# Optimization experiments

Hardware: AMD Instinct MI355X
Metric: run time of the kernel (lower is better)

Reference implementation:

```python
import jax, jax.numpy as jnp
import numpy as np

K = 32          # neighbors
DIV = 4         # division
S = K // DIV    # maxpool window
EPS = 1e-5      # BatchNorm eps (torch default)


def _bn_last(x, g, b):
    # BatchNorm over channel = last axis, training-mode batch stats (biased var),
    # equivalent to torch's transpose->BatchNorm2d->transpose in Dense(in_dim=4).
    m = x.mean(axis=(0, 1, 2), keepdims=True)
    v = x.var(axis=(0, 1, 2), keepdims=True)
    return (x - m) / jnp.sqrt(v + EPS) * g + b


def setup_inputs() -> dict:
    key = jax.random.key(0)
    ks = jax.random.split(key, 16)
    B, N, M, F1, F2 = 8, 4096, 2048, 128, 256
    Fmid = 64
    Cin = Fmid + F1  # 192
    inp = {
        "points": jax.random.normal(ks[0], (B, N, 3), dtype=jnp.float32),
        "queries": jax.random.normal(ks[1], (B, M, 3), dtype=jnp.float32),
        "prev_features": jax.random.normal(ks[2], (B, N, F1), dtype=jnp.float32),
        # dense1: 3 -> 32
        "g1": jnp.ones((3,), jnp.float32),
        "b1": jnp.zeros((3,), jnp.float32),
        "W1": jax.random.normal(ks[3], (3, Fmid // 2), dtype=jnp.float32) * 0.3,
        "c1": jnp.zeros((Fmid // 2,), jnp.float32),
        # dense2: 32 -> 64
        "g2": jnp.ones((Fmid // 2,), jnp.float32),
        "b2": jnp.zeros((Fmid // 2,), jnp.float32),
        "W2": jax.random.normal(ks[4], (Fmid // 2, Fmid), dtype=jnp.float32) * 0.1,
        "c2": jnp.zeros((Fmid,), jnp.float32),
        # conv block: BN2d(192) + Conv2d(192 -> 256, kernel (1,4))
        "g3": jnp.ones((Cin,), jnp.float32),
        "b3": jnp.zeros((Cin,), jnp.float32),
        "Wc": jax.random.normal(ks[5], (F2, Cin, DIV), dtype=jnp.float32) * 0.05,
        "bc": jnp.zeros((F2,), jnp.float32),
    }
    return inp


def reference(points, queries, prev_features, g1, b1, W1, c1, g2, b2, W2, c2,
              g3, b3, Wc, bc):
    B, N, _ = points.shape
    M = queries.shape[1]

    # --- KNN: negative squared distance, topk largest = k nearest ---
    # dist[b,m,n] = -||q-p||^2 = 2 q.p - ||q||^2 - ||p||^2
    dist = (2.0 * jnp.einsum('bmd,bnd->bmn', queries, points)
            - jnp.sum(queries ** 2, -1)[:, :, None]
            - jnp.sum(points ** 2, -1)[:, None, :])
    _, idx = jax.lax.top_k(dist, K)  # (B, M, K) int32

    gather = jax.vmap(lambda feats, i: feats[i])  # (N,F),(M,K) -> (M,K,F)
    knn_pts = gather(points, idx)                 # (B, M, K, 3)

    # local coords: center - neighbor
    local = queries[:, :, None, :] - knn_pts       # (B, M, K, 3)

    # dense1 / dense2: BN -> Linear -> ReLU
    h = jax.nn.relu(_bn_last(local, g1, b1) @ W1 + c1)  # (B,M,K,32)
    h = jax.nn.relu(_bn_last(h, g2, b2) @ W2 + c2)      # (B,M,K,64)

    # gather previous features, concat
    prev_k = gather(prev_features, idx)                 # (B,M,K,F1)
    feat = jnp.concatenate([h, prev_k], axis=-1)        # (B,M,K,192)

    # permute to NCHW, maxpool (1,S) stride S over K -> width DIV
    x = jnp.transpose(feat, (0, 3, 1, 2))               # (B,C,M,K)
    C = x.shape[1]
    x = x.reshape(B, C, M, DIV, S).max(axis=-1)         # (B,C,M,DIV)

    # BN2d over channel (training-mode batch stats)
    m = x.mean(axis=(0, 2, 3), keepdims=True)
    v = x.var(axis=(0, 2, 3), keepdims=True)
    x = (x - m) / jnp.sqrt(v + EPS) * g3[None, :, None, None] + b3[None, :, None, None]

    # Conv2d kernel (1,DIV) collapses width to 1: contraction over (C, DIV)
    out = jnp.einsum('bcmd,ocd->bmo', x, Wc) + bc       # (B,M,F2)
    return jax.nn.relu(out)
```

## Files before the change

### kernel.cpp

```cpp
#include <hip/hip_runtime.h>
#include <hip/hip_bf16.h>
#include <math.h>


#define B_   8
#define N_   4096
#define M_   2048
#define K_   32
#define F1_  128
#define F2_  256
#define CIN_ 192
#define NROWS_ (B_*M_*K_)
#define NQ_    (B_*M_)
#define EPS_ 1e-5f

#define S2_BLK 512
#define S3_BLK 128
#define S3_ROWS (65536 / S3_BLK)

typedef __attribute__((ext_vector_type(8))) short bf16x8;
typedef __attribute__((ext_vector_type(4))) float f32x4;

__device__ __forceinline__ unsigned int fkey(float qx, float qy, float qz, float qq,
                                             float x, float y, float z) {
    float dot = fmaf(qz, z, fmaf(qy, y, __fmul_rn(qx, x)));
    float pp  = __fadd_rn(__fadd_rn(__fmul_rn(x, x), __fmul_rn(y, y)), __fmul_rn(z, z));
    float d   = __fsub_rn(__fsub_rn(__fmul_rn(2.0f, dot), qq), pp);
    unsigned int u = __float_as_uint(d);
    return u ^ ((unsigned int)((int)u >> 31) | 0x80000000u);
}

__device__ __forceinline__ unsigned int pack_hi(float f0, float f1) {
    return (__float_as_uint(f0) >> 16) | (__float_as_uint(f1) & 0xFFFF0000u);
}
__device__ __forceinline__ unsigned int pack_lo(float f0, float f1) {
    float r0 = f0 - __uint_as_float(__float_as_uint(f0) & 0xFFFF0000u);
    float r1 = f1 - __uint_as_float(__float_as_uint(f1) & 0xFFFF0000u);
    return (__float_as_uint(r0) >> 16) | (__float_as_uint(r1) & 0xFFFF0000u);
}

__global__ __launch_bounds__(512) void knn_kernel(const float* __restrict__ points,
                                                  const float* __restrict__ queries,
                                                  int* __restrict__ idx_out,
                                                  float* __restrict__ local_out,
                                                  float* __restrict__ part1) {
    __shared__ float px[4160], py[4160], pz[4160];
    __shared__ float acc1[8][6];
    const int q0 = blockIdx.x * 8;
    const int b  = q0 >> 11;
    const float* pb = points + (size_t)b * N_ * 3;
    for (int p = threadIdx.x; p < N_; p += 512) {
        const float* g = pb + p * 3;
        int a = (p >> 6) * 65 + (p & 63);
        px[a] = g[0]; py[a] = g[1]; pz[a] = g[2];
    }
    __syncthreads();

    const int lane = threadIdx.x & 63;
    const int wid  = threadIdx.x >> 6;
    const int q = q0 + wid;
    const float qx = queries[q * 3 + 0];
    const float qy = queries[q * 3 + 1];
    const float qz = queries[q * 3 + 2];
    const float qq = __fadd_rn(__fadd_rn(__fmul_rn(qx, qx), __fmul_rn(qy, qy)), __fmul_rn(qz, qz));

    unsigned long long m0 = 0ull, m1 = 0ull;
    #pragma unroll 4
    for (unsigned int j = 0; j < 64; ++j) {
        int a = (int)j * 65 + lane;
        unsigned int fk = fkey(qx, qy, qz, qq, px[a], py[a], pz[a]);
        unsigned long long key = ((unsigned long long)fk << 32)
                               | (unsigned int)~((unsigned int)lane + (j << 6));
        if (key > m1) {
            unsigned long long lo = (key < m0) ? key : m0;
            m0 = (key > m0) ? key : m0;
            m1 = lo;
        }
    }

    unsigned long long takenT = 0ull;
    int sel_n = 0;
    const int rb = lane * 65;
    for (int r = 0; r < 32; ++r) {
        unsigned int m_fk = (unsigned int)(m0 >> 32);
        unsigned int g = m_fk;
        #pragma unroll
        for (int off = 32; off; off >>= 1) {
            unsigned int o = __shfl_xor(g, off, 64);
            g = (o > g) ? o : g;
        }
        unsigned long long mk = __ballot(m_fk == g);
        unsigned int nstar;
        if (__popcll(mk) == 1) {
            int src = __ffsll(mk) - 1;
            nstar = ~(unsigned int)__shfl((int)(unsigned int)m0, src, 64);
        } else {
            unsigned int nm = (m_fk == g) ? ~(unsigned int)m0 : 0xFFFFFFFFu;
            #pragma unroll
            for (int off = 32; off; off >>= 1) {
                unsigned int o = __shfl_xor(nm, off, 64);
                nm = (o < nm) ? o : nm;
            }
            nstar = nm;
        }
        if (lane == r) sel_n = (int)nstar;
        const int w  = nstar & 63;
        const int js = (int)(nstar >> 6);
        if (lane == js) takenT |= (1ull << w);
        if (lane == w) { m0 = m1; m1 = 0ull; }
        unsigned long long need = __ballot(lane == w && m0 == 0ull);
        if (need) {
            int a2 = rb + w;
            unsigned int fk2 = fkey(qx, qy, qz, qq, px[a2], py[a2], pz[a2]);
            if ((unsigned int)(takenT >> w) & 1u) fk2 = 0u;
            unsigned int g2 = fk2;
            #pragma unroll
            for (int off = 32; off; off >>= 1) {
                unsigned int o = __shfl_xor(g2, off, 64);
                g2 = (o > g2) ? o : g2;
            }
            unsigned long long mk2 = __ballot(fk2 == g2);
            int src2 = __ffsll(mk2) - 1;
            if (lane == w) {
                m0 = ((unsigned long long)g2 << 32)
                   | (unsigned int)~((unsigned int)w + ((unsigned int)src2 << 6));
            }
        }
    }

    float vx = 0.f, vy = 0.f, vz = 0.f;
    if (lane < 32) {
        idx_out[q * K_ + lane] = sel_n;
        int a = (sel_n >> 6) * 65 + (sel_n & 63);
        vx = __fsub_rn(qx, px[a]);
        vy = __fsub_rn(qy, py[a]);
        vz = __fsub_rn(qz, pz[a]);
        size_t o = ((size_t)q * K_ + lane) * 3;
        local_out[o + 0] = vx; local_out[o + 1] = vy; local_out[o + 2] = vz;
    }
    float s0 = vx, s1 = vy, s2 = vz, s3 = vx*vx, s4 = vy*vy, s5 = vz*vz;
    #pragma unroll
    for (int off = 32; off; off >>= 1) {
        s0 += __shfl_xor(s0, off, 64); s1 += __shfl_xor(s1, off, 64);
        s2 += __shfl_xor(s2, off, 64); s3 += __shfl_xor(s3, off, 64);
        s4 += __shfl_xor(s4, off, 64); s5 += __shfl_xor(s5, off, 64);
    }
    if (lane == 0) { acc1[wid][0]=s0; acc1[wid][1]=s1; acc1[wid][2]=s2;
                     acc1[wid][3]=s3; acc1[wid][4]=s4; acc1[wid][5]=s5; }
    __syncthreads();
    if (threadIdx.x < 6) {
        float s = 0.f;
        #pragma unroll
        for (int i = 0; i < 8; ++i) s += acc1[i][threadIdx.x];
        part1[blockIdx.x * 8 + threadIdx.x] = s;
    }
}

__global__ __launch_bounds__(256) void fold1_kernel(const float* __restrict__ part1,
                             const float* __restrict__ g1, const float* __restrict__ b1,
                             const float* __restrict__ W1, const float* __restrict__ c1,
                             float* __restrict__ W1p, float* __restrict__ c1p) {
    __shared__ float red[32][8];
    __shared__ float cs[8];
    const int t = threadIdx.x;
    const int c = t & 7, ch = t >> 3;
    float s = 0.f;
    for (int i = 0; i < 64; ++i) s += part1[(ch * 64 + i) * 8 + c];
    red[ch][c] = s;
    __syncthreads();
    if (t < 8) {
        float v = 0.f;
        #pragma unroll
        for (int i = 0; i < 32; ++i) v += red[i][t];
        cs[t] = v;
    }
    __syncthreads();
    if (t >= 32) return;
    const float inv_n = 1.0f / (float)NROWS_;
    float cacc = c1[t];
    #pragma unroll
    for (int c3 = 0; c3 < 3; ++c3) {
        float mean = cs[c3] * inv_n;
        float var  = cs[3 + c3] * inv_n - mean * mean;
        float sc   = g1[c3] / sqrtf(var + EPS_);
        float tc   = b1[c3] - mean * sc;
        float w    = W1[c3 * 32 + t];
        W1p[c3 * 32 + t] = sc * w;
        cacc += tc * w;
    }
    c1p[t] = cacc;
}

__global__ __launch_bounds__(256) void stats2_kernel(const float* __restrict__ local,
                                                     const float* __restrict__ W1p,
                                                     const float* __restrict__ c1p,
                                                     float* __restrict__ part2) {
    __shared__ float w[96], cb[32];
    __shared__ float red[4][64];
    if (threadIdx.x < 96) w[threadIdx.x] = W1p[threadIdx.x];
    if (threadIdx.x < 32) cb[threadIdx.x] = c1p[threadIdx.x];
    __syncthreads();
    float sum[32], sq[32];
    #pragma unroll
    for (int i = 0; i < 32; ++i) { sum[i] = 0.f; sq[i] = 0.f; }
    int tid = blockIdx.x * 256 + threadIdx.x;
    for (int r = tid; r < NROWS_; r += S2_BLK * 256) {
        float x = local[(size_t)r*3], y = local[(size_t)r*3+1], z = local[(size_t)r*3+2];
        #pragma unroll
        for (int f = 0; f < 32; ++f) {
            float h = fmaf(z, w[64 + f], fmaf(y, w[32 + f], fmaf(x, w[f], cb[f])));
            h = fmaxf(h, 0.0f);
            sum[f] += h; sq[f] += h * h;
        }
    }
    #pragma unroll
    for (int f = 0; f < 32; ++f) {
        #pragma unroll
        for (int off = 32; off; off >>= 1) {
            sum[f] += __shfl_xor(sum[f], off, 64);
            sq[f]  += __shfl_xor(sq[f], off, 64);
        }
    }
    int lane = threadIdx.x & 63, wid = threadIdx.x >> 6;
    if (lane == 0) {
        #pragma unroll
        for (int f = 0; f < 32; ++f) { red[wid][f] = sum[f]; red[wid][32 + f] = sq[f]; }
    }
    __syncthreads();
    if (threadIdx.x < 64) {
        part2[blockIdx.x * 64 + threadIdx.x] =
            red[0][threadIdx.x] + red[1][threadIdx.x] + red[2][threadIdx.x] + red[3][threadIdx.x];
    }
}

__global__ void fold2_kernel(const float* __restrict__ part2,
                             const float* __restrict__ g2, const float* __restrict__ b2,
                             const float* __restrict__ W2, const float* __restrict__ c2,
                             float* __restrict__ W2p, float* __restrict__ c2p) {
    __shared__ float cs[64];
    int f = threadIdx.x;
    {
        float s = 0.f;
        #pragma unroll 8
        for (int i = 0; i < S2_BLK; ++i) s += part2[i * 64 + f];
        cs[f] = s;
    }
    __syncthreads();
    const float inv_n = 1.0f / (float)NROWS_;
    float cacc = c2[f];
    for (int c = 0; c < 32; ++c) {
        float mean = cs[c] * inv_n;
        float var  = cs[32 + c] * inv_n - mean * mean;
        float sc   = g2[c] / sqrtf(var + EPS_);
        float tc   = b2[c] - mean * sc;
        float wv   = W2[c * 64 + f];
        W2p[c * 64 + f] = sc * wv;
        cacc += tc * wv;
    }
    c2p[f] = cacc;
}

__global__ __launch_bounds__(256) void h2pool_kernel(const float* __restrict__ local,
                                                     const float* __restrict__ W1p,
                                                     const float* __restrict__ c1p,
                                                     const float* __restrict__ W2p,
                                                     const float* __restrict__ c2p,
                                                     float* __restrict__ xp) {
    __shared__ float h1buf[4][32 * 32];
    const int lane = threadIdx.x & 63, wid = threadIdx.x >> 6;
    const int q = blockIdx.x * 4 + wid;

    float w2c[32];
    #pragma unroll 8
    for (int c = 0; c < 32; ++c) w2c[c] = W2p[c * 64 + lane];
    const float c2l = c2p[lane];

    const int f0 = lane & 31;
    const float wa = W1p[f0], wb = W1p[32 + f0], wc = W1p[64 + f0], cc = c1p[f0];
    float* hb = &h1buf[wid][0];
    #pragma unroll 2
    for (int i = 0; i < 16; ++i) {
        int t = lane + 64 * i;
        int k = t >> 5;
        size_t lo = ((size_t)q * K_ + k) * 3;
        float x = local[lo], y = local[lo + 1], z = local[lo + 2];
        float h = fmaf(z, wc, fmaf(y, wb, fmaf(x, wa, cc)));
        hb[t] = fmaxf(h, 0.0f);
    }
    __syncthreads();

    float pm[4] = {-INFINITY, -INFINITY, -INFINITY, -INFINITY};
    #pragma unroll 2
    for (int k = 0; k < 32; ++k) {
        const float* hk = &hb[k * 32];
        float acc = c2l;
        #pragma unroll
        for (int c = 0; c < 32; ++c) acc = fmaf(hk[c], w2c[c], acc);
        float h2 = fmaxf(acc, 0.0f);
        int g = k >> 3;
        pm[g] = fmaxf(pm[g], h2);
    }

    float* xq = xp + (size_t)q * 4 * CIN_;
    #pragma unroll
    for (int g = 0; g < 4; ++g) xq[g * CIN_ + lane] = pm[g];
}

__global__ __launch_bounds__(256) void gatherpool_kernel(const int* __restrict__ idx,
                                                         const float* __restrict__ prev,
                                                         float* __restrict__ xp) {
    const int lane = threadIdx.x & 63, wid = threadIdx.x >> 6;
    const int bid = blockIdx.x;
    const int q = ((bid & 7) << 11) + ((bid >> 3) << 2) + wid;
    const int b = q >> 11;

    int iv = 0;
    if (lane < 32) iv = idx[q * K_ + lane];
    float p0[4] = {-INFINITY, -INFINITY, -INFINITY, -INFINITY};
    float p1[4] = {-INFINITY, -INFINITY, -INFINITY, -INFINITY};
    const float* pbase = prev + (size_t)b * N_ * F1_;
    #pragma unroll 4
    for (int k = 0; k < 32; ++k) {
        int row = __shfl(iv, k, 64);
        const float* pr = pbase + (size_t)row * F1_;
        float v0 = pr[lane];
        float v1 = pr[64 + lane];
        int g = k >> 3;
        p0[g] = fmaxf(p0[g], v0);
        p1[g] = fmaxf(p1[g], v1);
    }

    float* xq = xp + (size_t)q * 4 * CIN_;
    #pragma unroll
    for (int g = 0; g < 4; ++g) {
        xq[g * CIN_ + 64 + lane]  = p0[g];
        xq[g * CIN_ + 128 + lane] = p1[g];
    }
}

__global__ __launch_bounds__(192) void stats3_kernel(const float* __restrict__ xp,
                                                     float* __restrict__ part3) {
    int c = threadIdx.x;
    int r0 = blockIdx.x * S3_ROWS;
    float s = 0.f, sq = 0.f;
    #pragma unroll 4
    for (int i = 0; i < S3_ROWS; ++i) {
        float v = xp[(size_t)(r0 + i) * CIN_ + c];
        s += v; sq += v * v;
    }
    part3[blockIdx.x * 384 + c]       = s;
    part3[blockIdx.x * 384 + 192 + c] = sq;
}

__global__ __launch_bounds__(384) void finalize3_kernel(const float* __restrict__ part3,
                                                        float* __restrict__ stats3) {
    int t = threadIdx.x;
    float s = 0.f;
    #pragma unroll 4
    for (int i = 0; i < S3_BLK; ++i) s += part3[i * 384 + t];
    stats3[t] = s;
}

__global__ __launch_bounds__(256) void fold3_kernel(const float* __restrict__ stats3,
                                                    const float* __restrict__ g3, const float* __restrict__ b3,
                                                    const float* __restrict__ Wc, const float* __restrict__ bc,
                                                    unsigned short* __restrict__ Wh,
                                                    unsigned short* __restrict__ Wl,
                                                    float* __restrict__ bcp) {
    const int o = blockIdx.x;
    const float inv_n = 1.0f / (float)(NQ_ * 4);
    __shared__ float red[256];
    float tacc = 0.f;
    for (int t = threadIdx.x; t < CIN_ * 4; t += 256) {
        int c = t >> 2, d = t & 3;
        float mean = stats3[c] * inv_n;
        float var  = stats3[192 + c] * inv_n - mean * mean;
        float sc   = g3[c] / sqrtf(var + EPS_);
        float tc   = b3[c] - mean * sc;
        float wv   = Wc[(size_t)o * (CIN_ * 4) + t];
        float w    = sc * wv;
        unsigned int u = __float_as_uint(w);
        float rr = w - __uint_as_float(u & 0xFFFF0000u);
        int f  = d * CIN_ + c;
        int ks = f >> 5, j = f & 7, lg = (f >> 3) & 3;
        size_t fi = ((size_t)(ks * 16 + (o >> 4)) * 64 + (lg * 16 + (o & 15))) * 8 + j;
        Wh[fi] = (unsigned short)(u >> 16);
        Wl[fi] = (unsigned short)(__float_as_uint(rr) >> 16);
        tacc += tc * wv;
    }
    red[threadIdx.x] = tacc;
    __syncthreads();
    for (int s = 128; s; s >>= 1) {
        if (threadIdx.x < s) red[threadIdx.x] += red[threadIdx.x + s];
        __syncthreads();
    }
    if (threadIdx.x == 0) bcp[o] = bc[o] + red[0];
}

__global__ __launch_bounds__(512) void conv_kernel(const float* __restrict__ xp,
                                                   const unsigned short* __restrict__ Wh,
                                                   const unsigned short* __restrict__ Wl,
                                                   const float* __restrict__ bcp,
                                                   float* __restrict__ out) {
    __shared__ __align__(16) unsigned short Ah_s[64 * 64];
    __shared__ __align__(16) unsigned short Al_s[64 * 64];
    __shared__ __align__(16) unsigned short Bh_s[2 * 16 * 64 * 8];
    __shared__ __align__(16) unsigned short Bl_s[2 * 16 * 64 * 8];

    const int tid  = threadIdx.x;
    const int lane = tid & 63;
    const int wid  = tid >> 6;
    const int wr   = wid >> 2;
    const int wc   = wid & 3;
    const int row0 = blockIdx.x * 64;

    f32x4 acc[2][4];
    #pragma unroll
    for (int i = 0; i < 2; ++i)
        #pragma unroll
        for (int n = 0; n < 4; ++n) acc[i][n] = (f32x4){0.f, 0.f, 0.f, 0.f};

    const int ar  = tid >> 3;
    const int akq = tid & 7;
    const int a_byte = ar * 128 + ((akq ^ (ar & 7)) << 4);
    const float* arow = xp + (size_t)(row0 + ar) * 768 + akq * 8;

    const int fr_row = lane & 15;
    const int fr_grp = lane >> 4;

    for (int ks2 = 0; ks2 < 12; ++ks2) {
        __syncthreads();
        {
            const float* p = arow + ks2 * 64;
            float4 v0 = *(const float4*)p;
            float4 v1 = *(const float4*)(p + 4);
            uint4 h4, l4;
            h4.x = pack_hi(v0.x, v0.y); h4.y = pack_hi(v0.z, v0.w);
            h4.z = pack_hi(v1.x, v1.y); h4.w = pack_hi(v1.z, v1.w);
            l4.x = pack_lo(v0.x, v0.y); l4.y = pack_lo(v0.z, v0.w);
            l4.z = pack_lo(v1.x, v1.y); l4.w = pack_lo(v1.z, v1.w);
            *(uint4*)((char*)Ah_s + a_byte) = h4;
            *(uint4*)((char*)Al_s + a_byte) = l4;
        }
        {
            const uint4* gh = (const uint4*)(Wh + (size_t)ks2 * 16384);
            const uint4* gl = (const uint4*)(Wl + (size_t)ks2 * 16384);
            uint4* lh = (uint4*)Bh_s;
            uint4* ll = (uint4*)Bl_s;
            #pragma unroll
            for (int i = 0; i < 4; ++i) {
                lh[tid + 512 * i] = gh[tid + 512 * i];
                ll[tid + 512 * i] = gl[tid + 512 * i];
            }
        }
        __syncthreads();
        #pragma unroll
        for (int ks = 0; ks < 2; ++ks) {
            bf16x8 ah[2], al[2];
            #pragma unroll
            for (int i = 0; i < 2; ++i) {
                int r = wr * 32 + i * 16 + fr_row;
                int slot = ks * 4 + fr_grp;
                int byte = r * 128 + ((slot ^ (r & 7)) << 4);
                ah[i] = *(const bf16x8*)((const char*)Ah_s + byte);
                al[i] = *(const bf16x8*)((const char*)Al_s + byte);
            }
            #pragma unroll
            for (int nt = 0; nt < 4; ++nt) {
                int bidx = ((ks * 16 + wc * 4 + nt) * 64 + lane) * 8;
                bf16x8 bh = *(const bf16x8*)(Bh_s + bidx);
                bf16x8 bl = *(const bf16x8*)(Bl_s + bidx);
                #pragma unroll
                for (int i = 0; i < 2; ++i) {
                    acc[i][nt] = __builtin_amdgcn_mfma_f32_16x16x32_bf16(ah[i], bh, acc[i][nt], 0, 0, 0);
                    acc[i][nt] = __builtin_amdgcn_mfma_f32_16x16x32_bf16(ah[i], bl, acc[i][nt], 0, 0, 0);
                    acc[i][nt] = __builtin_amdgcn_mfma_f32_16x16x32_bf16(al[i], bh, acc[i][nt], 0, 0, 0);
                }
            }
        }
    }

    float bias[4];
    #pragma unroll
    for (int nt = 0; nt < 4; ++nt) bias[nt] = bcp[wc * 64 + nt * 16 + fr_row];
    #pragma unroll
    for (int i = 0; i < 2; ++i) {
        #pragma unroll
        for (int nt = 0; nt < 4; ++nt) {
            int col = wc * 64 + nt * 16 + fr_row;
            #pragma unroll
            for (int rg = 0; rg < 4; ++rg) {
                int row = row0 + wr * 32 + i * 16 + fr_grp * 4 + rg;
                out[(size_t)row * F2_ + col] = fmaxf(acc[i][nt][rg] + bias[nt], 0.0f);
            }
        }
    }
}

extern "C" void kernel_launch(void* const* d_in, const int* in_sizes, int n_in,
                              void* d_out, int out_size, void* d_ws, size_t ws_size,
                              hipStream_t stream) {
    const float* points  = (const float*)d_in[0];
    const float* queries = (const float*)d_in[1];
    const float* prev    = (const float*)d_in[2];
    const float* g1 = (const float*)d_in[3];
    const float* b1 = (const float*)d_in[4];
    const float* W1 = (const float*)d_in[5];
    const float* c1 = (const float*)d_in[6];
    const float* g2 = (const float*)d_in[7];
    const float* b2 = (const float*)d_in[8];
    const float* W2 = (const float*)d_in[9];
    const float* c2 = (const float*)d_in[10];
    const float* g3 = (const float*)d_in[11];
    const float* b3 = (const float*)d_in[12];
    const float* Wc = (const float*)d_in[13];
    const float* bc = (const float*)d_in[14];
    float* out = (float*)d_out;

    char* ws = (char*)d_ws;
    size_t off_idx    = 0;
    size_t off_local  = off_idx + (size_t)NQ_*K_*4;
    size_t off_stats3 = off_local + (size_t)NROWS_*3*4;
    size_t off_W1p    = off_stats3 + 4096;
    size_t off_c1p    = off_W1p + 512;
    size_t off_W2p    = off_c1p + 512;
    size_t off_c2p    = off_W2p + 8192;
    size_t off_Wt     = off_c2p + 512;
    size_t off_bcp    = off_Wt + 786432;
    size_t off_xp     = off_bcp + 1024;

    int*   idx    = (int*)(ws + off_idx);
    float* local  = (float*)(ws + off_local);
    float* stats3 = (float*)(ws + off_stats3);
    float* W1p    = (float*)(ws + off_W1p);
    float* c1p    = (float*)(ws + off_c1p);
    float* W2p    = (float*)(ws + off_W2p);
    float* c2p    = (float*)(ws + off_c2p);
    unsigned short* Wh = (unsigned short*)(ws + off_Wt);
    unsigned short* Wl = (unsigned short*)(ws + off_Wt + 393216);
    float* bcp    = (float*)(ws + off_bcp);
    float* xp     = (float*)(ws + off_xp);
    float* part1  = (float*)(ws + off_Wt);
    float* part2  = (float*)(ws + off_Wt + 65536);
    float* part3  = (float*)(ws + off_local);

    knn_kernel<<<NQ_ / 8, 512, 0, stream>>>(points, queries, idx, local, part1);
    fold1_kernel<<<1, 256, 0, stream>>>(part1, g1, b1, W1, c1, W1p, c1p);
    stats2_kernel<<<S2_BLK, 256, 0, stream>>>(local, W1p, c1p, part2);
    fold2_kernel<<<1, 64, 0, stream>>>(part2, g2, b2, W2, c2, W2p, c2p);
    h2pool_kernel<<<NQ_ / 4, 256, 0, stream>>>(local, W1p, c1p, W2p, c2p, xp);
    gatherpool_kernel<<<NQ_ / 4, 256, 0, stream>>>(idx, prev, xp);
    stats3_kernel<<<S3_BLK, 192, 0, stream>>>(xp, part3);
    finalize3_kernel<<<1, 384, 0, stream>>>(part3, stats3);
    fold3_kernel<<<F2_, 256, 0, stream>>>(stats3, g3, b3, Wc, bc, Wh, Wl, bcp);
    conv_kernel<<<NQ_ / 64, 512, 0, stream>>>(xp, Wh, Wl, bcp, out);
}
```

Measured before the change: 420.6 us.

## Precompute point norms in KNN, widen reductions, tweak unrolls and stats3 grid

The KNN kernel now computes each point's squared norm once into shared memory, so the distance scan does one FMA and a subtract instead of recomputing the norm for every query. It also builds the key index with a decrementing counter. Separately, fold2 splits its partial-sum reduction across two waves, gatherpool unrolls more deeply, and stats3 launches 512 blocks of 128 rows instead of 128 blocks of 512 rows. The extra shared-memory array raises LDS use per KNN block, and finalize3 must now sum 512 partials; it still loops over S3_BLK, so it follows the new value.

```diff
diff --git a/kernel.cpp b/kernel.cpp
--- a/kernel.cpp
+++ b/kernel.cpp
@@ -15,17 +15,15 @@
 #define EPS_ 1e-5f
 
 #define S2_BLK 512
-#define S3_BLK 128
-#define S3_ROWS (65536 / S3_BLK)
+#define S3_BLK 512
 
 typedef __attribute__((ext_vector_type(8))) short bf16x8;
 typedef __attribute__((ext_vector_type(4))) float f32x4;
 
-__device__ __forceinline__ unsigned int fkey(float qx, float qy, float qz, float qq,
-                                             float x, float y, float z) {
+__device__ __forceinline__ unsigned int fkey_pp(float qx, float qy, float qz, float qq,
+                                                float x, float y, float z, float pv) {
     float dot = fmaf(qz, z, fmaf(qy, y, __fmul_rn(qx, x)));
-    float pp  = __fadd_rn(__fadd_rn(__fmul_rn(x, x), __fmul_rn(y, y)), __fmul_rn(z, z));
-    float d   = __fsub_rn(__fsub_rn(__fmul_rn(2.0f, dot), qq), pp);
+    float d   = __fsub_rn(fmaf(2.0f, dot, -qq), pv);
     unsigned int u = __float_as_uint(d);
     return u ^ ((unsigned int)((int)u >> 31) | 0x80000000u);
 }
@@ -44,15 +42,17 @@
                                                   int* __restrict__ idx_out,
                                                   float* __restrict__ local_out,
                                                   float* __restrict__ part1) {
-    __shared__ float px[4160], py[4160], pz[4160];
+    __shared__ float px[4160], py[4160], pz[4160], pp[4160];
     __shared__ float acc1[8][6];
     const int q0 = blockIdx.x * 8;
     const int b  = q0 >> 11;
     const float* pb = points + (size_t)b * N_ * 3;
     for (int p = threadIdx.x; p < N_; p += 512) {
         const float* g = pb + p * 3;
+        float x = g[0], y = g[1], z = g[2];
         int a = (p >> 6) * 65 + (p & 63);
-        px[a] = g[0]; py[a] = g[1]; pz[a] = g[2];
+        px[a] = x; py[a] = y; pz[a] = z;
+        pp[a] = __fadd_rn(__fadd_rn(__fmul_rn(x, x), __fmul_rn(y, y)), __fmul_rn(z, z));
     }
     __syncthreads();
 
@@ -65,12 +65,13 @@
     const float qq = __fadd_rn(__fadd_rn(__fmul_rn(qx, qx), __fmul_rn(qy, qy)), __fmul_rn(qz, qz));
 
     unsigned long long m0 = 0ull, m1 = 0ull;
-    #pragma unroll 4
-    for (unsigned int j = 0; j < 64; ++j) {
-        int a = (int)j * 65 + lane;
-        unsigned int fk = fkey(qx, qy, qz, qq, px[a], py[a], pz[a]);
-        unsigned long long key = ((unsigned long long)fk << 32)
-                               | (unsigned int)~((unsigned int)lane + (j << 6));
+    unsigned int klo = ~(unsigned int)lane;
+    #pragma unroll 8
+    for (int j = 0; j < 64; ++j) {
+        int a = j * 65 + lane;
+        unsigned int fk = fkey_pp(qx, qy, qz, qq, px[a], py[a], pz[a], pp[a]);
+        unsigned long long key = ((unsigned long long)fk << 32) | klo;
+        klo -= 64u;
         if (key > m1) {
             unsigned long long lo = (key < m0) ? key : m0;
             m0 = (key > m0) ? key : m0;
@@ -111,7 +112,7 @@
         unsigned long long need = __ballot(lane == w && m0 == 0ull);
         if (need) {
             int a2 = rb + w;
-            unsigned int fk2 = fkey(qx, qy, qz, qq, px[a2], py[a2], pz[a2]);
+            unsigned int fk2 = fkey_pp(qx, qy, qz, qq, px[a2], py[a2], pz[a2], pp[a2]);
             if ((unsigned int)(takenT >> w) & 1u) fk2 = 0u;
             unsigned int g2 = fk2;
             #pragma unroll
@@ -237,14 +238,20 @@
                              const float* __restrict__ g2, const float* __restrict__ b2,
                              const float* __restrict__ W2, const float* __restrict__ c2,
                              float* __restrict__ W2p, float* __restrict__ c2p) {
+    __shared__ float red2[2][64];
     __shared__ float cs[64];
-    int f = threadIdx.x;
+    int t = threadIdx.x;
+    int f = t & 63, h = t >> 6;
     {
         float s = 0.f;
         #pragma unroll 8
-        for (int i = 0; i < S2_BLK; ++i) s += part2[i * 64 + f];
-        cs[f] = s;
-    }
+        for (int i = h * (S2_BLK / 2); i < (h + 1) * (S2_BLK / 2); ++i)
+            s += part2[i * 64 + f];
+        red2[h][f] = s;
+    }
+    __syncthreads();
+    if (t >= 64) return;
+    cs[f] = red2[0][f] + red2[1][f];
     __syncthreads();
     const float inv_n = 1.0f / (float)NROWS_;
     float cacc = c2[f];
@@ -319,7 +326,7 @@
     float p0[4] = {-INFINITY, -INFINITY, -INFINITY, -INFINITY};
     float p1[4] = {-INFINITY, -INFINITY, -INFINITY, -INFINITY};
     const float* pbase = prev + (size_t)b * N_ * F1_;
-    #pragma unroll 4
+    #pragma unroll 8
     for (int k = 0; k < 32; ++k) {
         int row = __shfl(iv, k, 64);
         const float* pr = pbase + (size_t)row * F1_;
@@ -341,10 +348,10 @@
 __global__ __launch_bounds__(192) void stats3_kernel(const float* __restrict__ xp,
                                                      float* __restrict__ part3) {
     int c = threadIdx.x;
-    int r0 = blockIdx.x * S3_ROWS;
+    int r0 = blockIdx.x * 128;
     float s = 0.f, sq = 0.f;
     #pragma unroll 4
-    for (int i = 0; i < S3_ROWS; ++i) {
+    for (int i = 0; i < 128; ++i) {
         float v = xp[(size_t)(r0 + i) * CIN_ + c];
         s += v; sq += v * v;
     }
@@ -547,7 +554,7 @@
     knn_kernel<<<NQ_ / 8, 512, 0, stream>>>(points, queries, idx, local, part1);
     fold1_kernel<<<1, 256, 0, stream>>>(part1, g1, b1, W1, c1, W1p, c1p);
     stats2_kernel<<<S2_BLK, 256, 0, stream>>>(local, W1p, c1p, part2);
-    fold2_kernel<<<1, 64, 0, stream>>>(part2, g2, b2, W2, c2, W2p, c2p);
+    fold2_kernel<<<1, 128, 0, stream>>>(part2, g2, b2, W2, c2, W2p, c2p);
     h2pool_kernel<<<NQ_ / 4, 256, 0, stream>>>(local, W1p, c1p, W2p, c2p, xp);
     gatherpool_kernel<<<NQ_ / 4, 256, 0, stream>>>(idx, prev, xp);
     stats3_kernel<<<S3_BLK, 192, 0, stream>>>(xp, part3);
```

New measurement: 426.4 us. Within noise of the previous version (+1.4%).
